# Performance work log

Measured on AMD Instinct MI355X. Metric: run time of the kernel, lower is better.

## Reference

```python
import jax, jax.numpy as jnp
import numpy as np

B, S, D, H = 2, 2048, 1024, 16
HD = D // H  # head_dim = 64


def setup_inputs() -> dict:
    key = jax.random.key(0)
    k1, k2, k3 = jax.random.split(key, 3)
    inputs = jax.random.normal(k1, (B, S, D), dtype=jnp.float32)
    segment_positions = jnp.broadcast_to(jnp.arange(S, dtype=jnp.int32), (B, S))
    # causal boolean mask, broadcast over batch and heads: [1,1,S,S]
    mask = jnp.tril(jnp.ones((S, S), dtype=bool))[None, None]
    W_in = jax.random.normal(k2, (D, 3 * D), dtype=jnp.float32) * (D ** -0.5)
    W_out = jax.random.normal(k3, (D, D), dtype=jnp.float32) * (D ** -0.5)
    return {"inputs": inputs, "segment_positions": segment_positions,
            "mask": mask, "W_in": W_in, "W_out": W_out}


def _rope(x, pos):
    # x: [B,S,H,HD], pos: [B,S] int. Rotate-half RoPE with base 10000.
    half = HD // 2
    inv_freq = 1.0 / (10000.0 ** (jnp.arange(half, dtype=jnp.float32) / half))
    ang = pos[..., None].astype(jnp.float32) * inv_freq          # [B,S,half]
    cos = jnp.cos(ang)[:, :, None, :]                             # [B,S,1,half]
    sin = jnp.sin(ang)[:, :, None, :]
    x1, x2 = jnp.split(x, 2, axis=-1)
    return jnp.concatenate([x1 * cos - x2 * sin, x1 * sin + x2 * cos], axis=-1)


def reference(inputs, segment_positions, mask, W_in, W_out):
    # fused QKV projection: [B,S,3D] -> [B,S,H,3*HD] -> chunk into q,k,v
    qkv = (inputs @ W_in).reshape(B, S, H, 3 * HD)
    q, k, v = jnp.split(qkv, 3, axis=-1)                          # each [B,S,H,HD]
    q = _rope(q, segment_positions)
    k = _rope(k, segment_positions)
    q = q / jnp.sqrt(jnp.asarray(HD, q.dtype))
    scores = jnp.einsum('bqhd,bkhd->bhqk', q, k)                  # [B,H,S,S]
    big_neg = jnp.finfo(scores.dtype).min
    scores = jnp.where(mask, scores, big_neg)
    attn = jax.nn.softmax(scores, axis=-1)
    x = jnp.einsum('bhqk,bkhd->bqhd', attn, v).reshape(B, S, D)
    return x @ W_out
```

## Files before the change

### kernel.cpp

```cpp
#include <hip/hip_runtime.h>

typedef unsigned short u16;
typedef __bf16 bf16x8 __attribute__((ext_vector_type(8)));
typedef float f32x4 __attribute__((ext_vector_type(4)));

__device__ __forceinline__ float b2f(u16 x) {
    union { float f; unsigned u; } v; v.u = ((unsigned)x) << 16; return v.f;
}
__device__ __forceinline__ u16 f2b(float f) {
    union { float f; unsigned u; } v; v.f = f;
    unsigned u = v.u;
    return (u16)((u + 0x7FFFu + ((u >> 16) & 1u)) >> 16);
}
__device__ __forceinline__ unsigned pk2(float a, float b) {
    unsigned ua = __float_as_uint(a), ub = __float_as_uint(b);
    return (ub & 0xFFFF0000u) | (ua >> 16);
}
__device__ __forceinline__ f32x4 mfma_16x16x32(bf16x8 a, bf16x8 b, f32x4 c) {
    return __builtin_amdgcn_mfma_f32_16x16x32_bf16(a, b, c, 0, 0, 0);
}
__device__ __forceinline__ void gld_lds16(const u16* g, u16* l) {
    __builtin_amdgcn_global_load_lds(
        (const __attribute__((address_space(1))) unsigned int*)g,
        (__attribute__((address_space(3))) unsigned int*)l,
        16, 0, 0);
}

#define VSTRIDE 2080
#define LOG2E 1.44269504f

__global__ __launch_bounds__(256) void prep(const float* __restrict__ inputs,
                                            u16* __restrict__ inB,
                                            const float* __restrict__ W_in,
                                            u16* __restrict__ WtB,
                                            const float* __restrict__ W_out,
                                            u16* __restrict__ WotB) {
    __shared__ float T[32][33];
    const int bx = blockIdx.x;
    if (bx < 4096) {
        int i = (bx * 256 + threadIdx.x) * 4;
        float4 v = *(const float4*)(inputs + i);
        ushort4 o;
        o.x = f2b(v.x); o.y = f2b(v.y); o.z = f2b(v.z); o.w = f2b(v.w);
        *(ushort4*)(inB + i) = o;
        return;
    }
    const float* src; u16* dst; int R, C, c0, r0;
    if (bx < 7168) {
        int t = bx - 4096; src = W_in; dst = WtB; R = 1024; C = 3072;
        c0 = (t % 96) * 32; r0 = (t / 96) * 32;
    } else {
        int t = bx - 7168; src = W_out; dst = WotB; R = 1024; C = 1024;
        c0 = (t % 32) * 32; r0 = (t / 32) * 32;
    }
    int tr = threadIdx.x >> 5, tc = threadIdx.x & 31;
#pragma unroll
    for (int p = 0; p < 4; ++p)
        T[tr + p * 8][tc] = src[(size_t)(r0 + tr + p * 8) * C + c0 + tc];
    __syncthreads();
#pragma unroll
    for (int p = 0; p < 4; ++p)
        dst[(size_t)(c0 + tr + p * 8) * R + r0 + tc] = f2b(T[tc][tr + p * 8]);
}

template <int BM, bool F32OUT>
__global__ __launch_bounds__(256) void gemm_tn(const u16* __restrict__ A,
                                               const u16* __restrict__ Bt,
                                               void* __restrict__ Cv,
                                               int M, int N, int K) {
    __shared__ u16 As[2][BM * 32];
    __shared__ u16 Bs[2][128 * 32];
    const int tid = threadIdx.x;
    const int m0 = blockIdx.y * BM;
    const int n0 = blockIdx.x * 128;
    const int w = tid >> 6, lane = tid & 63;
    const int col16 = lane & 15, quad = lane >> 4;
    constexpr int MI = BM / 32;
    const int wm = (w >> 1) * (BM / 2), wn = (w & 1) * 64;
    const int srow = (lane >> 2), sseg = (lane & 3) * 8;

    f32x4 acc[MI][4];
#pragma unroll
    for (int i = 0; i < MI; ++i)
#pragma unroll
        for (int j = 0; j < 4; ++j) acc[i][j] = (f32x4){0.f, 0.f, 0.f, 0.f};

    if (BM == 128) {
#pragma unroll
        for (int cc = 0; cc < 2; ++cc) {
            int c = w * 2 + cc, row = c * 16 + srow;
            gld_lds16(A + (size_t)(m0 + row) * K + sseg, &As[0][c * 512 + lane * 8]);
            gld_lds16(Bt + (size_t)(n0 + row) * K + sseg, &Bs[0][c * 512 + lane * 8]);
        }
    } else {
        int row = w * 16 + srow;
        gld_lds16(A + (size_t)(m0 + row) * K + sseg, &As[0][w * 512 + lane * 8]);
#pragma unroll
        for (int cc = 0; cc < 2; ++cc) {
            int c = w * 2 + cc, rowb = c * 16 + srow;
            gld_lds16(Bt + (size_t)(n0 + rowb) * K + sseg, &Bs[0][c * 512 + lane * 8]);
        }
    }

    const int NK = K >> 5;
    for (int ki = 0; ki < NK; ++ki) {
        const int cur = ki & 1;
        asm volatile("s_waitcnt vmcnt(0)" ::: "memory");
        asm volatile("s_barrier" ::: "memory");

        if (ki + 1 < NK) {
            const int kt = (ki + 1) << 5;
            if (BM == 128) {
#pragma unroll
                for (int cc = 0; cc < 2; ++cc) {
                    int c = w * 2 + cc, row = c * 16 + srow;
                    gld_lds16(A + (size_t)(m0 + row) * K + kt + sseg, &As[cur ^ 1][c * 512 + lane * 8]);
                    gld_lds16(Bt + (size_t)(n0 + row) * K + kt + sseg, &Bs[cur ^ 1][c * 512 + lane * 8]);
                }
            } else {
                int row = w * 16 + srow;
                gld_lds16(A + (size_t)(m0 + row) * K + kt + sseg, &As[cur ^ 1][w * 512 + lane * 8]);
#pragma unroll
                for (int cc = 0; cc < 2; ++cc) {
                    int c = w * 2 + cc, rowb = c * 16 + srow;
                    gld_lds16(Bt + (size_t)(n0 + rowb) * K + kt + sseg, &Bs[cur ^ 1][c * 512 + lane * 8]);
                }
            }
        }

        bf16x8 af[MI], bfr[4];
#pragma unroll
        for (int i = 0; i < MI; ++i)
            af[i] = *(const bf16x8*)&As[cur][(wm + i * 16 + col16) * 32 + quad * 8];
#pragma unroll
        for (int j = 0; j < 4; ++j)
            bfr[j] = *(const bf16x8*)&Bs[cur][(wn + j * 16 + col16) * 32 + quad * 8];
#pragma unroll
        for (int i = 0; i < MI; ++i)
#pragma unroll
            for (int j = 0; j < 4; ++j)
                acc[i][j] = mfma_16x16x32(af[i], bfr[j], acc[i][j]);

        asm volatile("s_waitcnt lgkmcnt(0)" ::: "memory");
    }

#pragma unroll
    for (int i = 0; i < MI; ++i) {
#pragma unroll
        for (int r = 0; r < 4; ++r) {
            int m = m0 + wm + i * 16 + quad * 4 + r;
            if (F32OUT) {
                float* Crow = (float*)Cv + (size_t)m * N + n0 + wn;
#pragma unroll
                for (int j = 0; j < 4; ++j)
                    Crow[j * 16 + col16] = acc[i][j][r];
            } else {
                u16* Crow = (u16*)Cv + (size_t)m * N + n0 + wn;
#pragma unroll
                for (int j = 0; j < 4; ++j)
                    Crow[j * 16 + col16] = f2b(acc[i][j][r]);
            }
        }
    }
}

__global__ __launch_bounds__(256) void gemm_tn64(const u16* __restrict__ A,
                                                 const u16* __restrict__ Bt,
                                                 float* __restrict__ C,
                                                 int M, int N, int K) {
    __shared__ u16 As[2][64 * 64];
    __shared__ u16 Bs[2][64 * 64];
    const int tid = threadIdx.x;
    const int m0 = blockIdx.y * 64;
    const int n0 = blockIdx.x * 64;
    const int w = tid >> 6, lane = tid & 63;
    const int col16 = lane & 15, quad = lane >> 4;
    const int wm = (w >> 1) * 32, wn = (w & 1) * 32;
    const int sr = lane >> 3;
    const int sg = ((lane & 7) ^ sr) * 8;
    const int swz = (col16 & 7) << 3;

    f32x4 acc[2][2];
#pragma unroll
    for (int i = 0; i < 2; ++i)
#pragma unroll
        for (int j = 0; j < 2; ++j) acc[i][j] = (f32x4){0.f, 0.f, 0.f, 0.f};

#pragma unroll
    for (int i = 0; i < 2; ++i) {
        int c = w * 2 + i;
        gld_lds16(A + (size_t)(m0 + c * 8 + sr) * K + sg, &As[0][c * 512 + lane * 8]);
    }
#pragma unroll
    for (int i = 0; i < 2; ++i) {
        int c = w * 2 + i;
        gld_lds16(Bt + (size_t)(n0 + c * 8 + sr) * K + sg, &Bs[0][c * 512 + lane * 8]);
    }

    const int NK = K >> 6;
    for (int ki = 0; ki < NK; ++ki) {
        const int cur = ki & 1;
        asm volatile("s_waitcnt vmcnt(0)" ::: "memory");
        asm volatile("s_barrier" ::: "memory");

        if (ki + 1 < NK) {
            const int kt = (ki + 1) << 6;
#pragma unroll
            for (int i = 0; i < 2; ++i) {
                int c = w * 2 + i;
                gld_lds16(A + (size_t)(m0 + c * 8 + sr) * K + kt + sg, &As[cur ^ 1][c * 512 + lane * 8]);
            }
#pragma unroll
            for (int i = 0; i < 2; ++i) {
                int c = w * 2 + i;
                gld_lds16(Bt + (size_t)(n0 + c * 8 + sr) * K + kt + sg, &Bs[cur ^ 1][c * 512 + lane * 8]);
            }
        }

#pragma unroll
        for (int ks = 0; ks < 2; ++ks) {
            const int ko = (ks * 32 + quad * 8) ^ swz;
            bf16x8 af[2], bfr[2];
#pragma unroll
            for (int i = 0; i < 2; ++i)
                af[i] = *(const bf16x8*)&As[cur][(wm + i * 16 + col16) * 64 + ko];
#pragma unroll
            for (int j = 0; j < 2; ++j)
                bfr[j] = *(const bf16x8*)&Bs[cur][(wn + j * 16 + col16) * 64 + ko];
#pragma unroll
            for (int i = 0; i < 2; ++i)
#pragma unroll
                for (int j = 0; j < 2; ++j)
                    acc[i][j] = mfma_16x16x32(af[i], bfr[j], acc[i][j]);
        }

        asm volatile("s_waitcnt lgkmcnt(0)" ::: "memory");
    }

#pragma unroll
    for (int i = 0; i < 2; ++i) {
#pragma unroll
        for (int r = 0; r < 4; ++r) {
            int m = m0 + wm + i * 16 + quad * 4 + r;
            float* Crow = C + (size_t)m * N + n0 + wn;
#pragma unroll
            for (int j = 0; j < 2; ++j)
                Crow[j * 16 + col16] = acc[i][j][r];
        }
    }
}

__global__ __launch_bounds__(256) void rope_vt(const u16* __restrict__ qkv,
                                               const int* __restrict__ segpos,
                                               u16* __restrict__ Qh,
                                               u16* __restrict__ Kh,
                                               u16* __restrict__ Vt) {
    __shared__ u16 T[32][72];
    const int bx = blockIdx.x;
    if (bx < 1024) {
        int t = bx * 256 + threadIdx.x;
        int seg = t & 3;
        int h = (t >> 2) & 15;
        int row = t >> 6;
        float pos = (float)segpos[row];
        const u16* base = qkv + (size_t)row * 3072 + h * 192 + seg * 8;
        union { uint4 u; u16 s[8]; } q1, q2, k1, k2, oq1, oq2, ok1, ok2;
        q1.u = *(const uint4*)(base);
        q2.u = *(const uint4*)(base + 32);
        k1.u = *(const uint4*)(base + 64);
        k2.u = *(const uint4*)(base + 96);
        const float qs = 0.125f * LOG2E;
#pragma unroll
        for (int j = 0; j < 8; ++j) {
            int d = seg * 8 + j;
            float inv_freq = __expf(-(float)d * (9.210340371976184f / 32.0f));
            float ang = pos * inv_freq;
            float c = __cosf(ang), s = __sinf(ang);
            float a1 = b2f(q1.s[j]), a2 = b2f(q2.s[j]);
            float b1 = b2f(k1.s[j]), b2v = b2f(k2.s[j]);
            oq1.s[j] = f2b((a1 * c - a2 * s) * qs);
            oq2.s[j] = f2b((a1 * s + a2 * c) * qs);
            ok1.s[j] = f2b(b1 * c - b2v * s);
            ok2.s[j] = f2b(b1 * s + b2v * c);
        }
        int b = row >> 11, srow = row & 2047;
        size_t idx = ((size_t)(b * 16 + h) * 2048 + srow) * 64 + seg * 8;
        *(uint4*)&Qh[idx]      = oq1.u;
        *(uint4*)&Qh[idx + 32] = oq2.u;
        *(uint4*)&Kh[idx]      = ok1.u;
        *(uint4*)&Kh[idx + 32] = ok2.u;
        return;
    }
    int bxx = bx - 1024;
    int s0 = (bxx & 63) * 32;
    int bh = bxx >> 6;
    int b = bh >> 4, h = bh & 15;
    int t = threadIdx.x;
    {
        int r = t >> 3, seg = t & 7;
        const u16* src = qkv + (size_t)(b * 2048 + s0 + r) * 3072 + h * 192 + 128 + seg * 8;
        *(uint4*)&T[r][seg * 8] = *(const uint4*)src;
    }
    __syncthreads();
    {
        int d = t >> 2, ss = (t & 3) * 8;
        union { uint4 u; u16 s[8]; } w;
#pragma unroll
        for (int j = 0; j < 8; ++j) w.s[j] = T[ss + j][d];
        *(uint4*)(Vt + (size_t)bh * 64 * VSTRIDE + (size_t)d * VSTRIDE + s0 + ss) = w.u;
    }
}

#define FIXED_M2 34.6246561f

__device__ const int UTQ[27] = {6,7,8,9,10,11,12,13,13,14,14,15,15, 5,12, 4,11, 3,10, 2,9, 1,8,15, 0,7,14};
__device__ const int UK0[27] = {0,0,0,0,0,0,0,0,14,0,14,0,14, 0,14, 0,14, 0,14, 0,14, 0,14,28, 0,14,28};
__device__ const int UNC[27] = {14,14,14,14,14,14,14,14,14,14,14,14,14, 12,12, 10,10, 8,8, 6,6, 4,4,4, 2,2,2};
__device__ const int UPS[27] = {-1,0,1,2,3,4,5,6,7,8,9,10,11, -1,12, -1,13, -1,14, -1,15, -1,16,17, -1,18,19};
__device__ const int RUN[9]    = {2,2,2,2,2,2,2,3,3};
__device__ const int RUS[9][3] = {{0,18,-1},{1,16,-1},{2,15,-1},{3,14,-1},{4,13,-1},
                                  {5,12,-1},{6,7,-1},{8,9,19},{10,11,17}};

__global__ __launch_bounds__(256) void attn_v18(const u16* __restrict__ Qh,
                                                const u16* __restrict__ Kh,
                                                const u16* __restrict__ Vt,
                                                u16* __restrict__ X,
                                                float* __restrict__ Opart,
                                                float* __restrict__ Lpart) {
    __shared__ u16 Ks[2][64 * 64];
    __shared__ u16 Vs[2][64 * 64];
    __shared__ u16 Ps[4][32 * 64];
    __shared__ float lred[4][32];
    const int tid = threadIdx.x;
    const int w = tid >> 6, lane = tid & 63;
    const int col16 = lane & 15, quad = lane >> 4;
    const int raw = blockIdx.x;
    const int bsw = (raw & 7) * 108 + (raw >> 3);
    const int bh = bsw / 27;
    const int slot = bsw - bh * 27;
    const int tq = UTQ[slot];
    const int c0 = UK0[slot];
    const int nc = UNC[slot];
    const int ps = UPS[slot];
    const int q0 = tq * 128 + w * 32;
    const u16* Qp = Qh + (size_t)bh * 2048 * 64;
    const u16* Kp = Kh + (size_t)bh * 2048 * 64;
    const u16* Vp = Vt + (size_t)bh * 64 * VSTRIDE;
    u16* Pw = Ps[w];
    const int swz = (col16 & 7) << 3;

    bf16x8 qa[2][2];
#pragma unroll
    for (int t = 0; t < 2; ++t)
#pragma unroll
        for (int hf = 0; hf < 2; ++hf)
            qa[t][hf] = *(const bf16x8*)&Qp[(size_t)(q0 + t * 16 + col16) * 64 + hf * 32 + quad * 8];

    float l_acc[2] = {0.f, 0.f};
    f32x4 o[2][4];
#pragma unroll
    for (int t = 0; t < 2; ++t)
#pragma unroll
        for (int f = 0; f < 4; ++f) o[t][f] = (f32x4){0.f, 0.f, 0.f, 0.f};

    const int sr = lane >> 3;
    const int sg = ((lane & 7) ^ sr) * 8;

    {
        const int k0 = c0 * 64;
#pragma unroll
        for (int i = 0; i < 2; ++i) {
            int c = w * 2 + i;
            gld_lds16(Kp + (size_t)(k0 + c * 8 + sr) * 64 + sg, &Ks[0][c * 512 + lane * 8]);
        }
#pragma unroll
        for (int i = 0; i < 2; ++i) {
            int c = w * 2 + i;
            gld_lds16(Vp + (size_t)(c * 8 + sr) * VSTRIDE + k0 + sg, &Vs[0][c * 512 + lane * 8]);
        }
    }

    for (int ci = 0; ci < nc; ++ci) {
        const int cur = ci & 1;
        const u16* KsC = Ks[cur];
        const u16* VsC = Vs[cur];

        asm volatile("s_waitcnt vmcnt(0)" ::: "memory");
        asm volatile("s_barrier" ::: "memory");

        if (ci + 1 < nc) {
            const int k0n = (c0 + ci + 1) * 64;
            u16* Kd = Ks[cur ^ 1];
            u16* Vd = Vs[cur ^ 1];
#pragma unroll
            for (int i = 0; i < 2; ++i) {
                int c = w * 2 + i;
                gld_lds16(Kp + (size_t)(k0n + c * 8 + sr) * 64 + sg, Kd + c * 512 + lane * 8);
            }
#pragma unroll
            for (int i = 0; i < 2; ++i) {
                int c = w * 2 + i;
                gld_lds16(Vp + (size_t)(c * 8 + sr) * VSTRIDE + k0n + sg, Vd + c * 512 + lane * 8);
            }
        }

        const int k0 = (c0 + ci) * 64;

        f32x4 s[2][4];
#pragma unroll
        for (int t = 0; t < 2; ++t)
#pragma unroll
            for (int kt = 0; kt < 4; ++kt) s[t][kt] = (f32x4){0.f, 0.f, 0.f, 0.f};
#pragma unroll
        for (int kt = 0; kt < 4; ++kt) {
            const u16* kb = &KsC[(kt * 16 + col16) * 64];
            bf16x8 kf0 = *(const bf16x8*)&kb[(quad * 8) ^ swz];
            bf16x8 kf1 = *(const bf16x8*)&kb[(32 + quad * 8) ^ swz];
            s[0][kt] = mfma_16x16x32(kf0, qa[0][0], s[0][kt]);
            s[0][kt] = mfma_16x16x32(kf1, qa[0][1], s[0][kt]);
            s[1][kt] = mfma_16x16x32(kf0, qa[1][0], s[1][kt]);
            s[1][kt] = mfma_16x16x32(kf1, qa[1][1], s[1][kt]);
        }

        const bool domask = (k0 + 63 > q0);
#pragma unroll
        for (int t = 0; t < 2; ++t) {
            const int qg = q0 + t * 16 + col16;
            float rs = 0.f;
#pragma unroll
            for (int kt = 0; kt < 4; ++kt) {
                float p[4];
#pragma unroll
                for (int r = 0; r < 4; ++r) {
                    float sv = s[t][kt][r];
                    if (domask && (k0 + kt * 16 + quad * 4 + r > qg)) sv = -1e30f;
                    p[r] = __builtin_amdgcn_exp2f(sv - FIXED_M2);
                    rs += p[r];
                }
                unsigned* prow = (unsigned*)&Pw[(t * 16 + col16) * 64 + ((kt * 16 + quad * 4) ^ swz)];
                prow[0] = pk2(p[0], p[1]);
                prow[1] = pk2(p[2], p[3]);
            }
            l_acc[t] += rs;
        }
        asm volatile("s_waitcnt lgkmcnt(0)" ::: "memory");

#pragma unroll
        for (int ss = 0; ss < 2; ++ss) {
            const int ko = (ss * 32 + quad * 8) ^ swz;
            bf16x8 pf0 = *(const bf16x8*)&Pw[(col16) * 64 + ko];
            bf16x8 pf1 = *(const bf16x8*)&Pw[(16 + col16) * 64 + ko];
#pragma unroll
            for (int f = 0; f < 4; ++f) {
                bf16x8 vf = *(const bf16x8*)&VsC[(f * 16 + col16) * 64 + ko];
                o[0][f] = mfma_16x16x32(pf0, vf, o[0][f]);
                o[1][f] = mfma_16x16x32(pf1, vf, o[1][f]);
            }
        }
        asm volatile("s_waitcnt lgkmcnt(0)" ::: "memory");
    }

    float lt[2];
#pragma unroll
    for (int t = 0; t < 2; ++t) {
        float l = l_acc[t];
        l += __shfl_xor(l, 16);
        l += __shfl_xor(l, 32);
        lt[t] = l;
        if (quad == 0) lred[w][t * 16 + col16] = l;
    }
    asm volatile("s_waitcnt lgkmcnt(0)" ::: "memory");

    if (ps >= 0) {
        const int pg = bh * 20 + ps;
        float* Op = Opart + ((size_t)pg * 128 + w * 32) * 64;
#pragma unroll
        for (int t = 0; t < 2; ++t) {
#pragma unroll
            for (int r = 0; r < 4; ++r) {
                float* Crow = Op + (t * 16 + quad * 4 + r) * 64;
#pragma unroll
                for (int f = 0; f < 4; ++f)
                    Crow[f * 16 + col16] = o[t][f][r];
            }
        }
        if (quad == 0) {
            float* Lp = Lpart + (size_t)pg * 128 + w * 32;
#pragma unroll
            for (int t = 0; t < 2; ++t) Lp[t * 16 + col16] = lt[t];
        }
        return;
    }

    const int b = bh >> 4, h = bh & 15;
#pragma unroll
    for (int t = 0; t < 2; ++t) {
#pragma unroll
        for (int r = 0; r < 4; ++r) {
            float inv = 1.0f / lred[w][t * 16 + quad * 4 + r];
            int srow = q0 + t * 16 + quad * 4 + r;
            u16* Xp = X + ((size_t)(b * 2048 + srow)) * 1024 + h * 64;
#pragma unroll
            for (int f = 0; f < 4; ++f)
                Xp[f * 16 + col16] = f2b(o[t][f][r] * inv);
        }
    }
}

__global__ __launch_bounds__(256) void attn_reduce(const float* __restrict__ Opart,
                                                   const float* __restrict__ Lpart,
                                                   u16* __restrict__ X) {
    const int bh = blockIdx.x;
    const int ti = blockIdx.y;
    const int tq = 7 + ti;
    const int tid = threadIdx.x;
    const int b = bh >> 4, h = bh & 15;
    const int np = RUN[ti];
    const size_t g0 = (size_t)(bh * 20 + RUS[ti][0]);
    const size_t g1 = (size_t)(bh * 20 + RUS[ti][1]);
    const size_t g2 = (np > 2) ? (size_t)(bh * 20 + RUS[ti][2]) : 0;
    const float4* O0 = (const float4*)Opart + g0 * 2048;
    const float4* O1 = (const float4*)Opart + g1 * 2048;
    const float4* O2 = (const float4*)Opart + g2 * 2048;
#pragma unroll
    for (int i = 0; i < 8; ++i) {
        int e4 = i * 256 + tid;
        int q = e4 >> 4, d0 = (e4 & 15) * 4;
        float4 a = O0[e4];
        float4 c = O1[e4];
        a.x += c.x; a.y += c.y; a.z += c.z; a.w += c.w;
        float l = Lpart[g0 * 128 + q] + Lpart[g1 * 128 + q];
        if (np > 2) {
            float4 d = O2[e4];
            a.x += d.x; a.y += d.y; a.z += d.z; a.w += d.w;
            l += Lpart[g2 * 128 + q];
        }
        float inv = 1.0f / l;
        ushort4 ov;
        ov.x = f2b(a.x * inv); ov.y = f2b(a.y * inv);
        ov.z = f2b(a.z * inv); ov.w = f2b(a.w * inv);
        *(ushort4*)&X[((size_t)(b * 2048 + tq * 128 + q)) * 1024 + h * 64 + d0] = ov;
    }
}

extern "C" void kernel_launch(void* const* d_in, const int* in_sizes, int n_in,
                              void* d_out, int out_size, void* d_ws, size_t ws_size,
                              hipStream_t stream) {
    const float* inputs = (const float*)d_in[0];
    const int* segpos   = (const int*)d_in[1];
    const float* W_in   = (const float*)d_in[3];
    const float* W_out  = (const float*)d_in[4];
    float* out = (float*)d_out;

    u16* ws = (u16*)d_ws;
    u16* qkv   = ws;
    u16* x     = qkv;
    u16* inB   = qkv + 12582912 + 512;
    u16* WtB   = inB + 4194304 + 512;
    u16* WotB  = WtB + 3145728 + 512;
    u16* Qh    = WotB + 1048576 + 512;
    u16* Kh    = Qh + 4194304 + 512;
    u16* Vt    = Kh + 4194304 + 512;
    float* Opart = (float*)(ws + 8388608);
    float* Lpart = (float*)(ws + 8388608 + 10485760);

    prep<<<dim3(8192), 256, 0, stream>>>(inputs, inB, W_in, WtB, W_out, WotB);
    gemm_tn<128, false><<<dim3(24, 32), 256, 0, stream>>>(inB, WtB, qkv, 4096, 3072, 1024);
    rope_vt<<<dim3(3072), 256, 0, stream>>>(qkv, segpos, Qh, Kh, Vt);
    attn_v18<<<dim3(864), 256, 0, stream>>>(Qh, Kh, Vt, x, Opart, Lpart);
    attn_reduce<<<dim3(32, 9), 256, 0, stream>>>(Opart, Lpart, x);
    gemm_tn64<<<dim3(16, 64), 256, 0, stream>>>(x, WotB, out, 4096, 1024, 1024);
}
```

Before: 201.5 us.

## Use 8-wave blocks for QKV GEMM and attention kernels

Both the QKV projection GEMM and the attention kernel move from 256 to 512 threads per block, with each wave owning a smaller sub-tile (GEMM waves do 64x32, attention waves handle 16 query rows instead of 32). Each wave now issues one async global-to-LDS load per operand per stage instead of two. The aim is more waves per CU for latency hiding and less per-wave register pressure. The cost is less MFMA work per LDS fragment load and more barrier participants per iteration.

```diff
diff --git a/kernel.cpp b/kernel.cpp
--- a/kernel.cpp
+++ b/kernel.cpp
@@ -63,43 +63,30 @@
         dst[(size_t)(c0 + tr + p * 8) * R + r0 + tc] = f2b(T[tc][tr + p * 8]);
 }
 
-template <int BM, bool F32OUT>
-__global__ __launch_bounds__(256) void gemm_tn(const u16* __restrict__ A,
-                                               const u16* __restrict__ Bt,
-                                               void* __restrict__ Cv,
-                                               int M, int N, int K) {
-    __shared__ u16 As[2][BM * 32];
+__global__ __launch_bounds__(512) void gemm_tn8(const u16* __restrict__ A,
+                                                const u16* __restrict__ Bt,
+                                                u16* __restrict__ C,
+                                                int M, int N, int K) {
+    __shared__ u16 As[2][128 * 32];
     __shared__ u16 Bs[2][128 * 32];
     const int tid = threadIdx.x;
-    const int m0 = blockIdx.y * BM;
+    const int m0 = blockIdx.y * 128;
     const int n0 = blockIdx.x * 128;
     const int w = tid >> 6, lane = tid & 63;
     const int col16 = lane & 15, quad = lane >> 4;
-    constexpr int MI = BM / 32;
-    const int wm = (w >> 1) * (BM / 2), wn = (w & 1) * 64;
+    const int wm = (w >> 2) * 64, wn = (w & 3) * 32;
     const int srow = (lane >> 2), sseg = (lane & 3) * 8;
 
-    f32x4 acc[MI][4];
-#pragma unroll
-    for (int i = 0; i < MI; ++i)
-#pragma unroll
-        for (int j = 0; j < 4; ++j) acc[i][j] = (f32x4){0.f, 0.f, 0.f, 0.f};
-
-    if (BM == 128) {
-#pragma unroll
-        for (int cc = 0; cc < 2; ++cc) {
-            int c = w * 2 + cc, row = c * 16 + srow;
-            gld_lds16(A + (size_t)(m0 + row) * K + sseg, &As[0][c * 512 + lane * 8]);
-            gld_lds16(Bt + (size_t)(n0 + row) * K + sseg, &Bs[0][c * 512 + lane * 8]);
-        }
-    } else {
+    f32x4 acc[4][2];
+#pragma unroll
+    for (int i = 0; i < 4; ++i)
+#pragma unroll
+        for (int j = 0; j < 2; ++j) acc[i][j] = (f32x4){0.f, 0.f, 0.f, 0.f};
+
+    {
         int row = w * 16 + srow;
         gld_lds16(A + (size_t)(m0 + row) * K + sseg, &As[0][w * 512 + lane * 8]);
-#pragma unroll
-        for (int cc = 0; cc < 2; ++cc) {
-            int c = w * 2 + cc, rowb = c * 16 + srow;
-            gld_lds16(Bt + (size_t)(n0 + rowb) * K + sseg, &Bs[0][c * 512 + lane * 8]);
-        }
+        gld_lds16(Bt + (size_t)(n0 + row) * K + sseg, &Bs[0][w * 512 + lane * 8]);
     }
 
     const int NK = K >> 5;
@@ -110,56 +97,36 @@
 
         if (ki + 1 < NK) {
             const int kt = (ki + 1) << 5;
-            if (BM == 128) {
-#pragma unroll
-                for (int cc = 0; cc < 2; ++cc) {
-                    int c = w * 2 + cc, row = c * 16 + srow;
-                    gld_lds16(A + (size_t)(m0 + row) * K + kt + sseg, &As[cur ^ 1][c * 512 + lane * 8]);
-                    gld_lds16(Bt + (size_t)(n0 + row) * K + kt + sseg, &Bs[cur ^ 1][c * 512 + lane * 8]);
-                }
-            } else {
-                int row = w * 16 + srow;
-                gld_lds16(A + (size_t)(m0 + row) * K + kt + sseg, &As[cur ^ 1][w * 512 + lane * 8]);
-#pragma unroll
-                for (int cc = 0; cc < 2; ++cc) {
-                    int c = w * 2 + cc, rowb = c * 16 + srow;
-                    gld_lds16(Bt + (size_t)(n0 + rowb) * K + kt + sseg, &Bs[cur ^ 1][c * 512 + lane * 8]);
-                }
-            }
-        }
-
-        bf16x8 af[MI], bfr[4];
-#pragma unroll
-        for (int i = 0; i < MI; ++i)
+            int row = w * 16 + srow;
+            gld_lds16(A + (size_t)(m0 + row) * K + kt + sseg, &As[cur ^ 1][w * 512 + lane * 8]);
+            gld_lds16(Bt + (size_t)(n0 + row) * K + kt + sseg, &Bs[cur ^ 1][w * 512 + lane * 8]);
+        }
+
+        bf16x8 af[4], bfr[2];
+#pragma unroll
+        for (int i = 0; i < 4; ++i)
             af[i] = *(const bf16x8*)&As[cur][(wm + i * 16 + col16) * 32 + quad * 8];
 #pragma unroll
-        for (int j = 0; j < 4; ++j)
+        for (int j = 0; j < 2; ++j)
             bfr[j] = *(const bf16x8*)&Bs[cur][(wn + j * 16 + col16) * 32 + quad * 8];
 #pragma unroll
-        for (int i = 0; i < MI; ++i)
-#pragma unroll
-            for (int j = 0; j < 4; ++j)
+        for (int i = 0; i < 4; ++i)
+#pragma unroll
+            for (int j = 0; j < 2; ++j)
                 acc[i][j] = mfma_16x16x32(af[i], bfr[j], acc[i][j]);
 
         asm volatile("s_waitcnt lgkmcnt(0)" ::: "memory");
     }
 
 #pragma unroll
-    for (int i = 0; i < MI; ++i) {
+    for (int i = 0; i < 4; ++i) {
 #pragma unroll
         for (int r = 0; r < 4; ++r) {
             int m = m0 + wm + i * 16 + quad * 4 + r;
-            if (F32OUT) {
-                float* Crow = (float*)Cv + (size_t)m * N + n0 + wn;
-#pragma unroll
-                for (int j = 0; j < 4; ++j)
-                    Crow[j * 16 + col16] = acc[i][j][r];
-            } else {
-                u16* Crow = (u16*)Cv + (size_t)m * N + n0 + wn;
-#pragma unroll
-                for (int j = 0; j < 4; ++j)
-                    Crow[j * 16 + col16] = f2b(acc[i][j][r]);
-            }
+            u16* Crow = C + (size_t)m * N + n0 + wn;
+#pragma unroll
+            for (int j = 0; j < 2; ++j)
+                Crow[j * 16 + col16] = f2b(acc[i][j][r]);
         }
     }
 }
@@ -321,7 +288,7 @@
 __device__ const int RUS[9][3] = {{0,18,-1},{1,16,-1},{2,15,-1},{3,14,-1},{4,13,-1},
                                   {5,12,-1},{6,7,-1},{8,9,19},{10,11,17}};
 
-__global__ __launch_bounds__(256) void attn_v18(const u16* __restrict__ Qh,
+__global__ __launch_bounds__(512) void attn_v19(const u16* __restrict__ Qh,
                                                 const u16* __restrict__ Kh,
                                                 const u16* __restrict__ Vt,
                                                 u16* __restrict__ X,
@@ -329,8 +296,8 @@
                                                 float* __restrict__ Lpart) {
     __shared__ u16 Ks[2][64 * 64];
     __shared__ u16 Vs[2][64 * 64];
-    __shared__ u16 Ps[4][32 * 64];
-    __shared__ float lred[4][32];
+    __shared__ u16 Ps[8][16 * 64];
+    __shared__ float lred[8][16];
     const int tid = threadIdx.x;
     const int w = tid >> 6, lane = tid & 63;
     const int col16 = lane & 15, quad = lane >> 4;
@@ -342,42 +309,30 @@
     const int c0 = UK0[slot];
     const int nc = UNC[slot];
     const int ps = UPS[slot];
-    const int q0 = tq * 128 + w * 32;
+    const int q0 = tq * 128 + w * 16;
     const u16* Qp = Qh + (size_t)bh * 2048 * 64;
     const u16* Kp = Kh + (size_t)bh * 2048 * 64;
     const u16* Vp = Vt + (size_t)bh * 64 * VSTRIDE;
     u16* Pw = Ps[w];
     const int swz = (col16 & 7) << 3;
 
-    bf16x8 qa[2][2];
-#pragma unroll
-    for (int t = 0; t < 2; ++t)
-#pragma unroll
-        for (int hf = 0; hf < 2; ++hf)
-            qa[t][hf] = *(const bf16x8*)&Qp[(size_t)(q0 + t * 16 + col16) * 64 + hf * 32 + quad * 8];
-
-    float l_acc[2] = {0.f, 0.f};
-    f32x4 o[2][4];
-#pragma unroll
-    for (int t = 0; t < 2; ++t)
-#pragma unroll
-        for (int f = 0; f < 4; ++f) o[t][f] = (f32x4){0.f, 0.f, 0.f, 0.f};
+    bf16x8 qa[2];
+#pragma unroll
+    for (int hf = 0; hf < 2; ++hf)
+        qa[hf] = *(const bf16x8*)&Qp[(size_t)(q0 + col16) * 64 + hf * 32 + quad * 8];
+
+    float l_acc = 0.f;
+    f32x4 o[4];
+#pragma unroll
+    for (int f = 0; f < 4; ++f) o[f] = (f32x4){0.f, 0.f, 0.f, 0.f};
 
     const int sr = lane >> 3;
     const int sg = ((lane & 7) ^ sr) * 8;
 
     {
         const int k0 = c0 * 64;
-#pragma unroll
-        for (int i = 0; i < 2; ++i) {
-            int c = w * 2 + i;
-            gld_lds16(Kp + (size_t)(k0 + c * 8 + sr) * 64 + sg, &Ks[0][c * 512 + lane * 8]);
-        }
-#pragma unroll
-        for (int i = 0; i < 2; ++i) {
-            int c = w * 2 + i;
-            gld_lds16(Vp + (size_t)(c * 8 + sr) * VSTRIDE + k0 + sg, &Vs[0][c * 512 + lane * 8]);
-        }
+        gld_lds16(Kp + (size_t)(k0 + w * 8 + sr) * 64 + sg, &Ks[0][w * 512 + lane * 8]);
+        gld_lds16(Vp + (size_t)(w * 8 + sr) * VSTRIDE + k0 + sg, &Vs[0][w * 512 + lane * 8]);
     }
 
     for (int ci = 0; ci < nc; ++ci) {
@@ -390,120 +345,95 @@
 
         if (ci + 1 < nc) {
             const int k0n = (c0 + ci + 1) * 64;
-            u16* Kd = Ks[cur ^ 1];
-            u16* Vd = Vs[cur ^ 1];
-#pragma unroll
-            for (int i = 0; i < 2; ++i) {
-                int c = w * 2 + i;
-                gld_lds16(Kp + (size_t)(k0n + c * 8 + sr) * 64 + sg, Kd + c * 512 + lane * 8);
-            }
-#pragma unroll
-            for (int i = 0; i < 2; ++i) {
-                int c = w * 2 + i;
-                gld_lds16(Vp + (size_t)(c * 8 + sr) * VSTRIDE + k0n + sg, Vd + c * 512 + lane * 8);
-            }
+            gld_lds16(Kp + (size_t)(k0n + w * 8 + sr) * 64 + sg, &Ks[cur ^ 1][w * 512 + lane * 8]);
+            gld_lds16(Vp + (size_t)(w * 8 + sr) * VSTRIDE + k0n + sg, &Vs[cur ^ 1][w * 512 + lane * 8]);
         }
 
         const int k0 = (c0 + ci) * 64;
 
-        f32x4 s[2][4];
-#pragma unroll
-        for (int t = 0; t < 2; ++t)
-#pragma unroll
-            for (int kt = 0; kt < 4; ++kt) s[t][kt] = (f32x4){0.f, 0.f, 0.f, 0.f};
+        f32x4 s[4];
+#pragma unroll
+        for (int kt = 0; kt < 4; ++kt) s[kt] = (f32x4){0.f, 0.f, 0.f, 0.f};
 #pragma unroll
         for (int kt = 0; kt < 4; ++kt) {
             const u16* kb = &KsC[(kt * 16 + col16) * 64];
             bf16x8 kf0 = *(const bf16x8*)&kb[(quad * 8) ^ swz];
             bf16x8 kf1 = *(const bf16x8*)&kb[(32 + quad * 8) ^ swz];
-            s[0][kt] = mfma_16x16x32(kf0, qa[0][0], s[0][kt]);
-            s[0][kt] = mfma_16x16x32(kf1, qa[0][1], s[0][kt]);
-            s[1][kt] = mfma_16x16x32(kf0, qa[1][0], s[1][kt]);
-            s[1][kt] = mfma_16x16x32(kf1, qa[1][1], s[1][kt]);
+            s[kt] = mfma_16x16x32(kf0, qa[0], s[kt]);
+            s[kt] = mfma_16x16x32(kf1, qa[1], s[kt]);
         }
 
         const bool domask = (k0 + 63 > q0);
-#pragma unroll
-        for (int t = 0; t < 2; ++t) {
-            const int qg = q0 + t * 16 + col16;
+        {
+            const int qg = q0 + col16;
             float rs = 0.f;
 #pragma unroll
             for (int kt = 0; kt < 4; ++kt) {
                 float p[4];
 #pragma unroll
                 for (int r = 0; r < 4; ++r) {
-                    float sv = s[t][kt][r];
+                    float sv = s[kt][r];
                     if (domask && (k0 + kt * 16 + quad * 4 + r > qg)) sv = -1e30f;
                     p[r] = __builtin_amdgcn_exp2f(sv - FIXED_M2);
                     rs += p[r];
                 }
-                unsigned* prow = (unsigned*)&Pw[(t * 16 + col16) * 64 + ((kt * 16 + quad * 4) ^ swz)];
+                unsigned* prow = (unsigned*)&Pw[col16 * 64 + ((kt * 16 + quad * 4) ^ swz)];
                 prow[0] = pk2(p[0], p[1]);
                 prow[1] = pk2(p[2], p[3]);
             }
-            l_acc[t] += rs;
+            l_acc += rs;
         }
         asm volatile("s_waitcnt lgkmcnt(0)" ::: "memory");
 
 #pragma unroll
         for (int ss = 0; ss < 2; ++ss) {
             const int ko = (ss * 32 + quad * 8) ^ swz;
-            bf16x8 pf0 = *(const bf16x8*)&Pw[(col16) * 64 + ko];
-            bf16x8 pf1 = *(const bf16x8*)&Pw[(16 + col16) * 64 + ko];
+            bf16x8 pf = *(const bf16x8*)&Pw[col16 * 64 + ko];
 #pragma unroll
             for (int f = 0; f < 4; ++f) {
                 bf16x8 vf = *(const bf16x8*)&VsC[(f * 16 + col16) * 64 + ko];
-                o[0][f] = mfma_16x16x32(pf0, vf, o[0][f]);
-                o[1][f] = mfma_16x16x32(pf1, vf, o[1][f]);
+                o[f] = mfma_16x16x32(pf, vf, o[f]);
             }
         }
         asm volatile("s_waitcnt lgkmcnt(0)" ::: "memory");
     }
 
-    float lt[2];
-#pragma unroll
-    for (int t = 0; t < 2; ++t) {
-        float l = l_acc[t];
+    float lt;
+    {
+        float l = l_acc;
         l += __shfl_xor(l, 16);
         l += __shfl_xor(l, 32);
-        lt[t] = l;
-        if (quad == 0) lred[w][t * 16 + col16] = l;
+        lt = l;
+        if (quad == 0) lred[w][col16] = l;
     }
     asm volatile("s_waitcnt lgkmcnt(0)" ::: "memory");
 
     if (ps >= 0) {
         const int pg = bh * 20 + ps;
-        float* Op = Opart + ((size_t)pg * 128 + w * 32) * 64;
-#pragma unroll
-        for (int t = 0; t < 2; ++t) {
-#pragma unroll
-            for (int r = 0; r < 4; ++r) {
-                float* Crow = Op + (t * 16 + quad * 4 + r) * 64;
-#pragma unroll
-                for (int f = 0; f < 4; ++f)
-                    Crow[f * 16 + col16] = o[t][f][r];
-            }
+        float* Op = Opart + ((size_t)pg * 128 + w * 16) * 64;
+#pragma unroll
+        for (int r = 0; r < 4; ++r) {
+            float* Crow = Op + (quad * 4 + r) * 64;
+#pragma unroll
+            for (int f = 0; f < 4; ++f)
+                Crow[f * 16 + col16] = o[f][r];
         }
         if (quad == 0) {
-            float* Lp = Lpart + (size_t)pg * 128 + w * 32;
-#pragma unroll
-            for (int t = 0; t < 2; ++t) Lp[t * 16 + col16] = lt[t];
+            float* Lp = Lpart + (size_t)pg * 128 + w * 16;
+            Lp[col16] = lt;
         }
         return;
     }
 
     const int b = bh >> 4, h = bh & 15;
 #pragma unroll
-    for (int t = 0; t < 2; ++t) {
-#pragma unroll
-        for (int r = 0; r < 4; ++r) {
-            float inv = 1.0f / lred[w][t * 16 + quad * 4 + r];
-            int srow = q0 + t * 16 + quad * 4 + r;
-            u16* Xp = X + ((size_t)(b * 2048 + srow)) * 1024 + h * 64;
-#pragma unroll
-            for (int f = 0; f < 4; ++f)
-                Xp[f * 16 + col16] = f2b(o[t][f][r] * inv);
-        }
+    for (int r = 0; r < 4; ++r) {
+        float inv = 1.0f / lred[w][quad * 4 + r];
+        int srow = q0 + quad * 4 + r;
+        u16* Xp = X + ((size_t)(b * 2048 + srow)) * 1024 + h * 64;
+#pragma unroll
+        for (int f = 0; f < 4; ++f)
+            Xp[f * 16 + col16] = f2b(o[f][r] * inv);
     }
 }
 
@@ -565,9 +495,9 @@
     float* Lpart = (float*)(ws + 8388608 + 10485760);
 
     prep<<<dim3(8192), 256, 0, stream>>>(inputs, inB, W_in, WtB, W_out, WotB);
-    gemm_tn<128, false><<<dim3(24, 32), 256, 0, stream>>>(inB, WtB, qkv, 4096, 3072, 1024);
+    gemm_tn8<<<dim3(24, 32), 512, 0, stream>>>(inB, WtB, qkv, 4096, 3072, 1024);
     rope_vt<<<dim3(3072), 256, 0, stream>>>(qkv, segpos, Qh, Kh, Vt);
-    attn_v18<<<dim3(864), 256, 0, stream>>>(Qh, Kh, Vt, x, Opart, Lpart);
+    attn_v19<<<dim3(864), 512, 0, stream>>>(Qh, Kh, Vt, x, Opart, Lpart);
     attn_reduce<<<dim3(32, 9), 256, 0, stream>>>(Opart, Lpart, x);
     gemm_tn64<<<dim3(16, 64), 256, 0, stream>>>(x, WotB, out, 4096, 1024, 1024);
 }
```

Measured after the change: 198.8 us. No clear change (-1.3%).
